# Kernel tuning notes

Hardware: AMD Instinct MI355X
Metric: run time of the kernel (lower is better)

Reference implementation:

```python
import jax, jax.numpy as jnp
import numpy as np

HADAMARD_DIM = 4096  # power of 2 -> had_rem_dim is None, rem_dim = 1


def _fwht(x):
    """Fast Walsh-Hadamard transform along last dim (natural/Sylvester order).

    x: [B, n] with n a power of 2. Returns x @ H_n (unnormalized).
    Mirrors QuaRot's recursive butterfly: at each stage, pairs are split into
    (a+b) and (a-b) halves. log2(n) stages, each O(n) work per row.
    """
    bsz, n = x.shape
    steps = int(np.log2(n))
    u = x[:, :, None]  # [B, n, 1]
    m = n
    for _ in range(steps):  # fixed-trip loop over log2(n) stages, jit-friendly
        u = u.reshape(bsz, m // 2, 2, -1)
        a = u[:, :, 0, :]
        b = u[:, :, 1, :]
        u = jnp.concatenate([a + b, a - b], axis=-1)  # [B, m//2, 2k]
        m //= 2
    return u.reshape(bsz, n)


def matmul_hadU(x):
    """QuaRot matmul_hadU for power-of-2 dim: normalized FWHT, 1/sqrt(n)."""
    n = x.shape[-1]
    flat = x.reshape(-1, n)
    out = _fwht(flat) * (1.0 / np.sqrt(n))
    return out.reshape(x.shape).astype(x.dtype)


def setup_inputs() -> dict:
    key = jax.random.key(0)
    x = jax.random.normal(key, (8192, HADAMARD_DIM), dtype=jnp.float32)
    return {"x": x}


def reference(x):
    # FWHT.forward: x -> matmul_hadU_cuda(x, None, 1) -> cast back to x.dtype
    return matmul_hadU(x)
```

## Files before the change

kernel.cpp:

```cpp
#include <hip/hip_runtime.h>


#define N        4096
#define THREADS  256
#define A_STR    20
#define B_STR    328
#define LDS_FLOATS (B_STR * 15 + A_STR * 15 + 16)

__device__ __forceinline__ void fwht16(float v[16]) {
#pragma unroll
    for (int s = 1; s < 16; s <<= 1) {
#pragma unroll
        for (int k = 0; k < 16; k++) {
            if ((k & s) == 0) {
                float a = v[k];
                float b = v[k + s];
                v[k]     = a + b;
                v[k + s] = a - b;
            }
        }
    }
}

__global__ __launch_bounds__(THREADS)
void FWHT_83476984365427_kernel(const float* __restrict__ x,
                                float* __restrict__ out,
                                int nrows) {
    __shared__ float lds[LDS_FLOATS];

    const int row = blockIdx.x;
    if (row >= nrows) return;

    const float* __restrict__ xr  = x   + (size_t)row * N;
    float* __restrict__       otr = out + (size_t)row * N;
    const int t = threadIdx.x;

    float v[16];

    {
        const float4* xv = (const float4*)xr + (size_t)t * 4;
#pragma unroll
        for (int c = 0; c < 4; c++) {
            float4 f = xv[c];
            v[4 * c + 0] = f.x;
            v[4 * c + 1] = f.y;
            v[4 * c + 2] = f.z;
            v[4 * c + 3] = f.w;
        }
    }
    fwht16(v);

    {
        const int i2 = t >> 4;
        const int i1 = t & 15;
        float* dst = &lds[A_STR * i1 + B_STR * i2];
#pragma unroll
        for (int c = 0; c < 4; c++) {
            float4 f;
            f.x = v[4 * c + 0];
            f.y = v[4 * c + 1];
            f.z = v[4 * c + 2];
            f.w = v[4 * c + 3];
            *(float4*)(dst + 4 * c) = f;
        }
    }
    __syncthreads();

    {
        const int i2 = t >> 4;
        const int i0 = t & 15;
        const int base = i0 + B_STR * i2;
#pragma unroll
        for (int k = 0; k < 16; k++) v[k] = lds[base + A_STR * k];
        fwht16(v);
#pragma unroll
        for (int k = 0; k < 16; k++) lds[base + A_STR * k] = v[k];
    }
    __syncthreads();

    {
        const int i1 = t >> 4;
        const int i0 = t & 15;
        const int base = i0 + A_STR * i1;
#pragma unroll
        for (int k = 0; k < 16; k++) v[k] = lds[base + B_STR * k];
        fwht16(v);
        const float scale = 1.0f / 64.0f;
#pragma unroll
        for (int k = 0; k < 16; k++) otr[k * 256 + t] = v[k] * scale;
    }
}

extern "C" void kernel_launch(void* const* d_in, const int* in_sizes, int n_in,
                              void* d_out, int out_size, void* d_ws, size_t ws_size,
                              hipStream_t stream) {
    (void)n_in; (void)d_ws; (void)ws_size; (void)out_size;
    const float* x = (const float*)d_in[0];
    float* out = (float*)d_out;
    const int nrows = in_sizes[0] / N;
    dim3 grid(nrows);
    dim3 block(THREADS);
    FWHT_83476984365427_kernel<<<grid, block, 0, stream>>>(x, out, nrows);
}
```

Baseline: 227.0 us.

## Restructure FWHT as two radix-64 passes with one-wavefront blocks

```diff
diff --git a/kernel.cpp b/kernel.cpp
--- a/kernel.cpp
+++ b/kernel.cpp
@@ -2,16 +2,15 @@
 
 
 #define N        4096
-#define THREADS  256
-#define A_STR    20
-#define B_STR    328
-#define LDS_FLOATS (B_STR * 15 + A_STR * 15 + 16)
+#define THREADS  64
+#define TSTR     68
+#define LDS_FLOATS (64 * TSTR)
 
-__device__ __forceinline__ void fwht16(float v[16]) {
+__device__ __forceinline__ void fwht64(float v[64]) {
 #pragma unroll
-    for (int s = 1; s < 16; s <<= 1) {
+    for (int s = 1; s < 64; s <<= 1) {
 #pragma unroll
-        for (int k = 0; k < 16; k++) {
+        for (int k = 0; k < 64; k++) {
             if ((k & s) == 0) {
                 float a = v[k];
                 float b = v[k + s];
@@ -26,21 +25,21 @@
 void FWHT_83476984365427_kernel(const float* __restrict__ x,
                                 float* __restrict__ out,
                                 int nrows) {
-    __shared__ float lds[LDS_FLOATS];
+    __shared__ float tile[LDS_FLOATS];
 
     const int row = blockIdx.x;
     if (row >= nrows) return;
 
     const float* __restrict__ xr  = x   + (size_t)row * N;
     float* __restrict__       otr = out + (size_t)row * N;
-    const int t = threadIdx.x;
+    const int l = threadIdx.x;
 
-    float v[16];
+    float v[64];
 
     {
-        const float4* xv = (const float4*)xr + (size_t)t * 4;
+        const float4* xv = (const float4*)xr + (size_t)l * 16;
 #pragma unroll
-        for (int c = 0; c < 4; c++) {
+        for (int c = 0; c < 16; c++) {
             float4 f = xv[c];
             v[4 * c + 0] = f.x;
             v[4 * c + 1] = f.y;
@@ -48,14 +47,13 @@
             v[4 * c + 3] = f.w;
         }
     }
-    fwht16(v);
+
+    fwht64(v);
 
     {
-        const int i2 = t >> 4;
-        const int i1 = t & 15;
-        float* dst = &lds[A_STR * i1 + B_STR * i2];
+        float* dst = &tile[l * TSTR];
 #pragma unroll
-        for (int c = 0; c < 4; c++) {
+        for (int c = 0; c < 16; c++) {
             float4 f;
             f.x = v[4 * c + 0];
             f.y = v[4 * c + 1];
@@ -66,29 +64,14 @@
     }
     __syncthreads();
 
-    {
-        const int i2 = t >> 4;
-        const int i0 = t & 15;
-        const int base = i0 + B_STR * i2;
 #pragma unroll
-        for (int k = 0; k < 16; k++) v[k] = lds[base + A_STR * k];
-        fwht16(v);
+    for (int m = 0; m < 64; m++) v[m] = tile[m * TSTR + l];
+
+    fwht64(v);
+
+    const float scale = 1.0f / 64.0f;
 #pragma unroll
-        for (int k = 0; k < 16; k++) lds[base + A_STR * k] = v[k];
-    }
-    __syncthreads();
-
-    {
-        const int i1 = t >> 4;
-        const int i0 = t & 15;
-        const int base = i0 + A_STR * i1;
-#pragma unroll
-        for (int k = 0; k < 16; k++) v[k] = lds[base + B_STR * k];
-        fwht16(v);
-        const float scale = 1.0f / 64.0f;
-#pragma unroll
-        for (int k = 0; k < 16; k++) otr[k * 256 + t] = v[k] * scale;
-    }
+    for (int m = 0; m < 64; m++) otr[m * 64 + l] = v[m] * scale;
 }
 
 extern "C" void kernel_launch(void* const* d_in, const int* in_sizes, int n_in,
```

Result: no change. 230.1 us (+1.4%).
